# Kernel tuning notes

Hardware: AMD Instinct MI355X
Metric: run time of the kernel (lower is better)

## Reference

```python
import jax, jax.numpy as jnp
import numpy as np

B, C, N, M_MODES, EMB = 8, 64, 2048, 32, 256
MFREQ = 2 * M_MODES * (2 * M_MODES - 1)  # 4032
SCALE = 1.0 / (C * C)


def setup_inputs() -> dict:
    key = jax.random.key(0)
    ks = jax.random.split(key, 16)
    d = {
        "x": jax.random.normal(ks[0], (B, C, N), jnp.float32),
        "emb": jax.random.normal(ks[1], (B, EMB), jnp.float32),
        "Vf_re": jax.random.normal(ks[2], (MFREQ, N), jnp.float32),
        "Vf_im": jax.random.normal(ks[3], (MFREQ, N), jnp.float32),
        "Vi_re": jax.random.normal(ks[4], (N, MFREQ), jnp.float32),
        "Vi_im": jax.random.normal(ks[5], (N, MFREQ), jnp.float32),
        "w1_re": SCALE * jax.random.uniform(ks[6], (C, C, M_MODES, M_MODES), jnp.float32),
        "w1_im": SCALE * jax.random.uniform(ks[7], (C, C, M_MODES, M_MODES), jnp.float32),
        "w2_re": SCALE * jax.random.uniform(ks[8], (C, C, M_MODES, M_MODES), jnp.float32),
        "w2_im": SCALE * jax.random.uniform(ks[9], (C, C, M_MODES, M_MODES), jnp.float32),
        "m1_re": SCALE * jax.random.uniform(ks[10], (1, M_MODES, M_MODES, EMB), jnp.float32),
        "m1_im": SCALE * jax.random.uniform(ks[11], (1, M_MODES, M_MODES, EMB), jnp.float32),
        "m2_re": SCALE * jax.random.uniform(ks[12], (1, M_MODES, M_MODES, EMB), jnp.float32),
        "m2_im": SCALE * jax.random.uniform(ks[13], (1, M_MODES, M_MODES, EMB), jnp.float32),
    }
    return d


def _spectral_conv(x, emb, Vf, Vi, w1, w2, mod1, mod2):
    m = M_MODES
    # nuft.forward: [B,N,C] complex -> [B,MFREQ,C]
    xc = jnp.transpose(x, (0, 2, 1)).astype(jnp.complex64)
    x_nfft = jnp.einsum('mn,bnc->bmc', Vf, xc)
    # [B,C,2m,2m-1]
    x_ft = jnp.transpose(x_nfft, (0, 2, 1)).reshape(x.shape[0], C, 2 * m, 2 * m - 1)
    embc = emb.astype(jnp.complex64)[:, None, None, :]  # [B,1,1,EMB]
    phi1 = jnp.sum(mod1 * embc, axis=-1)  # [B,m,m]
    phi2 = jnp.sum(mod2 * embc, axis=-1)
    out1 = jnp.einsum('bixy,ioxy->boxy', x_ft[:, :, :m, :m], w1)
    out2 = jnp.einsum('bixy,ioxy->boxy', x_ft[:, :, -m:, :m], w2)
    mod1b = phi1[:, None, :, :] * out1
    mod2b = phi2[:, None, :, :] * out2
    out_ft = jnp.concatenate([mod1b, mod2b], axis=2)  # [B,C,2m,m]
    xf = out_ft.reshape(x.shape[0], C, 2 * m * m)
    # Hermitian-symmetry reconstruction: flip over mode AND channel dims, conj
    xf2 = jnp.conj(jnp.flip(xf[..., 2 * m:], axis=(-2, -1)))
    xf = jnp.concatenate([xf, xf2], axis=-1)  # [B,C,MFREQ]
    xf = jnp.transpose(xf, (0, 2, 1))  # [B,MFREQ,C]
    out = jnp.einsum('nm,bmc->bnc', Vi, xf)  # nuft.inverse -> [B,N,C]
    out = jnp.transpose(out, (0, 2, 1)) / N * 2
    return out.real


def reference(x, emb, Vf_re, Vf_im, Vi_re, Vi_im, w1_re, w1_im, w2_re, w2_im, m1_re, m1_im, m2_re, m2_im):
    Vf = Vf_re + 1j * Vf_im
    Vi = Vi_re + 1j * Vi_im
    w1 = w1_re + 1j * w1_im
    w2 = w2_re + 1j * w2_im
    mod1 = m1_re + 1j * m1_im
    mod2 = m2_re + 1j * m2_im
    return _spectral_conv(x, emb, Vf, Vi, w1, w2, mod1, mod2)
```

## Files before the change

### kernel.cpp

```cpp
#include <hip/hip_runtime.h>

#define BB    8
#define CC    64
#define NN    2048
#define GG    2048
#define MFREQ 4032

typedef __attribute__((ext_vector_type(4))) float f32x4;
typedef __attribute__((ext_vector_type(8))) short bf16x8;

static __device__ __forceinline__ unsigned short f2bf(float f) {
    union { float f; unsigned u; } v; v.f = f;
    unsigned r = v.u + 0x7fff + ((v.u >> 16) & 1);
    return (unsigned short)(r >> 16);
}

#define ASYNC_COPY16(gp, lp)                                                        \
    __builtin_amdgcn_global_load_lds(                                               \
        (const __attribute__((address_space(1))) unsigned int*)(gp),                \
        (__attribute__((address_space(3))) unsigned int*)(lp), 16, 0, 0)

__global__ __launch_bounds__(256) void prep_all(const float* __restrict__ vf_re,
                                                const float* __restrict__ vf_im,
                                                const float* __restrict__ x,
                                                const float* __restrict__ vi_re,
                                                const float* __restrict__ vi_im,
                                                const float* __restrict__ w1_re,
                                                const float* __restrict__ w1_im,
                                                const float* __restrict__ w2_re,
                                                const float* __restrict__ w2_im,
                                                const float* __restrict__ m1_re,
                                                const float* __restrict__ m1_im,
                                                const float* __restrict__ m2_re,
                                                const float* __restrict__ m2_im,
                                                const float* __restrict__ emb,
                                                unsigned short* __restrict__ af,
                                                unsigned short* __restrict__ xb,
                                                unsigned short* __restrict__ mi,
                                                unsigned int* __restrict__ wt,
                                                float* __restrict__ phi_re,
                                                float* __restrict__ phi_im) {
    __shared__ float sre[32][33];
    __shared__ float sim[32][33];
    __shared__ float sr4[4], si4[4];
    int blk = blockIdx.x;
    int t = threadIdx.x;

    if (blk < 6400) {
        float4 v[2][2];
        unsigned short* dst[2];
        if (blk < 2048) {
            #pragma unroll
            for (int u = 0; u < 2; ++u) {
                int gi = blk * 512 + u * 256 + t;
                int m = gi >> 8;
                int q8 = (gi & 255) * 8;
                int g = m & 2047;
                int f = (g >> 5) * 63 + (g & 31);
                const float* src = (m < 2048 ? vf_re : vf_im) + (size_t)f * 2048 + q8;
                v[u][0] = *(const float4*)src;
                v[u][1] = *(const float4*)(src + 4);
                dst[u] = af + (size_t)m * 2048 + q8;
            }
        } else if (blk < 2304) {
            #pragma unroll
            for (int u = 0; u < 2; ++u) {
                int gi = (blk - 2048) * 512 + u * 256 + t;
                int q8 = gi * 8;
                v[u][0] = *(const float4*)(x + q8);
                v[u][1] = *(const float4*)(x + q8 + 4);
                dst[u] = xb + q8;
            }
        } else {
            #pragma unroll
            for (int u = 0; u < 2; ++u) {
                int gi = (blk - 2304) * 512 + u * 256 + t;
                int n = gi >> 10;
                int q8 = (gi & 1023) * 8;
                int region = q8 >> 11;
                int off = q8 & 2047;
                if (region == 0) {
                    const float* src = vi_re + (size_t)n * MFREQ + off;
                    v[u][0] = *(const float4*)src;
                    v[u][1] = *(const float4*)(src + 4);
                } else if (region == 1) {
                    const float* src = vi_im + (size_t)n * MFREQ + off;
                    float4 a = *(const float4*)src;
                    float4 b = *(const float4*)(src + 4);
                    v[u][0].x = -a.x; v[u][0].y = -a.y; v[u][0].z = -a.z; v[u][0].w = -a.w;
                    v[u][1].x = -b.x; v[u][1].y = -b.y; v[u][1].z = -b.z; v[u][1].w = -b.w;
                } else {
                    if (off < 64) {
                        v[u][0].x = v[u][0].y = v[u][0].z = v[u][0].w = 0.0f;
                        v[u][1].x = v[u][1].y = v[u][1].z = v[u][1].w = 0.0f;
                    } else {
                        const float* src = (region == 2 ? vi_re : vi_im) + (size_t)n * MFREQ;
                        float4 a = *(const float4*)(src + 4092 - off);
                        float4 b = *(const float4*)(src + 4088 - off);
                        v[u][0].x = a.w; v[u][0].y = a.z; v[u][0].z = a.y; v[u][0].w = a.x;
                        v[u][1].x = b.w; v[u][1].y = b.z; v[u][1].z = b.y; v[u][1].w = b.x;
                    }
                }
                dst[u] = mi + (size_t)n * 8192 + q8;
            }
        }
        #pragma unroll
        for (int u = 0; u < 2; ++u) {
            uint4 o;
            o.x = (unsigned int)f2bf(v[u][0].x) | ((unsigned int)f2bf(v[u][0].y) << 16);
            o.y = (unsigned int)f2bf(v[u][0].z) | ((unsigned int)f2bf(v[u][0].w) << 16);
            o.z = (unsigned int)f2bf(v[u][1].x) | ((unsigned int)f2bf(v[u][1].y) << 16);
            o.w = (unsigned int)f2bf(v[u][1].z) | ((unsigned int)f2bf(v[u][1].w) << 16);
            *(uint4*)dst[u] = o;
        }
    } else if (blk < 14592) {
        int bi = blk - 6400;
        int wsel = bi >> 12;
        int bj = bi & 4095;
        int io0 = (bj >> 5) * 32;
        int xy0 = (bj & 31) * 32;
        const float* wre = wsel ? w2_re : w1_re;
        const float* wim = wsel ? w2_im : w1_im;
        int r = t >> 3, c4 = (t & 7) * 4;
        float4 a = *(const float4*)(wre + (size_t)(io0 + r) * 1024 + xy0 + c4);
        float4 b = *(const float4*)(wim + (size_t)(io0 + r) * 1024 + xy0 + c4);
        sre[r][c4 + 0] = a.x; sre[r][c4 + 1] = a.y; sre[r][c4 + 2] = a.z; sre[r][c4 + 3] = a.w;
        sim[r][c4 + 0] = b.x; sim[r][c4 + 1] = b.y; sim[r][c4 + 2] = b.z; sim[r][c4 + 3] = b.w;
        __syncthreads();
        int gr = t >> 3, ic4 = (t & 7) * 4;
        uint4 o;
        o.x = (unsigned int)f2bf(sre[ic4 + 0][gr]) | ((unsigned int)f2bf(sim[ic4 + 0][gr]) << 16);
        o.y = (unsigned int)f2bf(sre[ic4 + 1][gr]) | ((unsigned int)f2bf(sim[ic4 + 1][gr]) << 16);
        o.z = (unsigned int)f2bf(sre[ic4 + 2][gr]) | ((unsigned int)f2bf(sim[ic4 + 2][gr]) << 16);
        o.w = (unsigned int)f2bf(sre[ic4 + 3][gr]) | ((unsigned int)f2bf(sim[ic4 + 3][gr]) << 16);
        int g = xy0 + gr + wsel * 1024;
        *(uint4*)(wt + (size_t)g * 4096 + io0 + ic4) = o;
    } else {
        int g = blk - 14592, e = t;
        int xy = g & 1023;
        const float* mr = (g < 1024 ? m1_re : m2_re) + xy * 256;
        const float* mp = (g < 1024 ? m1_im : m2_im) + xy * 256;
        float vr = mr[e], vi = mp[e];
        for (int bb = 0; bb < 8; ++bb) {
            float em = emb[bb * 256 + e];
            float pr = vr * em, pi = vi * em;
            for (int s = 32; s > 0; s >>= 1) { pr += __shfl_down(pr, s); pi += __shfl_down(pi, s); }
            int wid = e >> 6;
            if ((e & 63) == 0) { sr4[wid] = pr; si4[wid] = pi; }
            __syncthreads();
            if (e == 0) {
                phi_re[bb * 2048 + g] = sr4[0] + sr4[1] + sr4[2] + sr4[3];
                phi_im[bb * 2048 + g] = si4[0] + si4[1] + si4[2] + si4[3];
            }
            __syncthreads();
        }
    }
}

template<int TM>
__global__ __launch_bounds__(256, 2) void gemm_sk(const unsigned short* __restrict__ A,
                                                  const unsigned short* __restrict__ Bm,
                                                  float* __restrict__ P,
                                                  int M, int N, int K, int Kper, int ilv) {
    constexpr int FI = TM / 32;
    __shared__ unsigned short As[TM * 64];
    __shared__ unsigned short Bs[TM * 64];
    int t = threadIdx.x;
    int lane = t & 63, w = t >> 6;
    int m0 = blockIdx.y * TM, n0 = blockIdx.x * TM;
    int z = blockIdx.z;
    int kbase = z * Kper;
    int wm = (w >> 1) * (TM / 2), wn = (w & 1) * (TM / 2);
    int lr = lane & 15, quad = lane >> 4;
    int rsub = lane >> 3, slot = lane & 7;

    f32x4 acc[FI][FI] = {};

    for (int kk = kbase; kk < kbase + Kper; kk += 64) {
        __syncthreads();
        #pragma unroll
        for (int l = 0; l < FI; ++l) {
            int r = (w * FI + l) * 8 + rsub;
            int c = slot ^ (r & 7);
            ASYNC_COPY16(A + (size_t)(m0 + r) * K + kk + c * 8, As + r * 64 + slot * 8);
            ASYNC_COPY16(Bm + (size_t)(n0 + r) * K + kk + c * 8, Bs + r * 64 + slot * 8);
        }
        __syncthreads();
        #pragma unroll
        for (int ks = 0; ks < 2; ++ks) {
            bf16x8 af[FI], bfr[FI];
            #pragma unroll
            for (int i = 0; i < FI; ++i) {
                int row = wm + i * 16 + lr;
                int q = (ks * 4 + quad) ^ (row & 7);
                af[i] = *(const bf16x8*)(As + row * 64 + q * 8);
                int rowb = wn + i * 16 + lr;
                int qb = (ks * 4 + quad) ^ (rowb & 7);
                bfr[i] = *(const bf16x8*)(Bs + rowb * 64 + qb * 8);
            }
            #pragma unroll
            for (int i = 0; i < FI; ++i)
            #pragma unroll
            for (int j = 0; j < FI; ++j)
                acc[i][j] = __builtin_amdgcn_mfma_f32_16x16x32_bf16(af[i], bfr[j], acc[i][j], 0, 0, 0);
        }
    }
    float* Pz = P + (size_t)z * M * N;
    size_t rstride = ilv ? 1024 : (size_t)N;
    #pragma unroll
    for (int i = 0; i < FI; ++i)
    #pragma unroll
    for (int j = 0; j < FI; ++j) {
        int rr = m0 + wm + i * 16 + quad * 4;
        int cc = n0 + wn + j * 16 + lr;
        size_t base = ilv ? ((size_t)(rr & 2047) * 1024 + cc * 2 + (rr >> 11))
                          : ((size_t)rr * N + cc);
        float* cp = Pz + base;
        f32x4 v = acc[i][j];
        cp[0]           = v.x;
        cp[rstride]     = v.y;
        cp[2 * rstride] = v.z;
        cp[3 * rstride] = v.w;
    }
}

__global__ __launch_bounds__(256) void reduce_k(const float* __restrict__ P,
                                                float* __restrict__ out,
                                                int S, size_t elems, float alpha) {
    size_t idx = ((size_t)blockIdx.x * 256 + threadIdx.x) * 4;
    float4 s = *(const float4*)(P + idx);
    for (int zz = 1; zz < S; ++zz) {
        float4 v = *(const float4*)(P + (size_t)zz * elems + idx);
        s.x += v.x; s.y += v.y; s.z += v.z; s.w += v.w;
    }
    s.x *= alpha; s.y *= alpha; s.z *= alpha; s.w *= alpha;
    *(float4*)(out + idx) = s;
}

__global__ __launch_bounds__(256, 4) void middle_k(const float* __restrict__ O1,
                                                   const unsigned int* __restrict__ wt,
                                                   const float* __restrict__ phi_re,
                                                   const float* __restrict__ phi_im,
                                                   unsigned short* __restrict__ Yt) {
    __shared__ unsigned int sW[2][4096];
    __shared__ float sInc[2][1024];
    int t = threadIdx.x;
    int g0 = blockIdx.x * 2;
    int b = t >> 5, p = t & 31;

    #pragma unroll
    for (int gt = 0; gt < 2; ++gt) {
        int g = g0 + gt;
        #pragma unroll
        for (int j = 0; j < 4; ++j)
            ASYNC_COPY16(wt + (size_t)g * 4096 + (j * 256 + t) * 4, &sW[gt][(j * 256 + t) * 4]);
        ASYNC_COPY16(O1 + (size_t)g * 1024 + t * 4, &sInc[gt][t * 4]);
    }
    __syncthreads();

    unsigned short reA[2][2], imA[2][2];

    #pragma unroll
    for (int gt = 0; gt < 2; ++gt) {
        int g = g0 + gt;
        float ar0 = 0.f, ai0 = 0.f, ar1 = 0.f, ai1 = 0.f;
        const float2* incp = (const float2*)sInc[gt] + b * 64;
        const unsigned int* wp = sW[gt] + 2 * p;
        #pragma unroll 8
        for (int i = 0; i < 64; ++i) {
            float2 a = incp[i];
            uint2 uu = *(const uint2*)(wp + i * 64);
            float w0r = __uint_as_float(uu.x << 16);
            float w0i = __uint_as_float(uu.x & 0xffff0000u);
            float w1r = __uint_as_float(uu.y << 16);
            float w1i = __uint_as_float(uu.y & 0xffff0000u);
            ar0 += a.x * w0r - a.y * w0i;  ai0 += a.x * w0i + a.y * w0r;
            ar1 += a.x * w1r - a.y * w1i;  ai1 += a.x * w1i + a.y * w1r;
        }
        float pr = phi_re[b * 2048 + g], pi = phi_im[b * 2048 + g];
        reA[0][gt] = f2bf(pr * ar0 - pi * ai0);
        imA[0][gt] = f2bf(pr * ai0 + pi * ar0);
        reA[1][gt] = f2bf(pr * ar1 - pi * ai1);
        imA[1][gt] = f2bf(pr * ai1 + pi * ar1);
    }

    #pragma unroll
    for (int ch = 0; ch < 2; ++ch) {
        int c = 2 * p + ch;
        size_t r0 = (size_t)(b * 64 + c) * 8192;
        size_t rf = (size_t)(b * 64 + 63 - c) * 8192;
        unsigned int ure = (unsigned int)reA[ch][0] | ((unsigned int)reA[ch][1] << 16);
        unsigned int uim = (unsigned int)imA[ch][0] | ((unsigned int)imA[ch][1] << 16);
        *(unsigned int*)(Yt + r0 + g0)        = ure;
        *(unsigned int*)(Yt + r0 + 2048 + g0) = uim;
        *(unsigned int*)(Yt + rf + 4096 + g0) = ure;
        *(unsigned int*)(Yt + rf + 6144 + g0) = uim;
    }
}

extern "C" void kernel_launch(void* const* d_in, const int* in_sizes, int n_in,
                              void* d_out, int out_size, void* d_ws, size_t ws_size,
                              hipStream_t stream) {
    const float* x     = (const float*)d_in[0];
    const float* emb   = (const float*)d_in[1];
    const float* vf_re = (const float*)d_in[2];
    const float* vf_im = (const float*)d_in[3];
    const float* vi_re = (const float*)d_in[4];
    const float* vi_im = (const float*)d_in[5];
    const float* w1_re = (const float*)d_in[6];
    const float* w1_im = (const float*)d_in[7];
    const float* w2_re = (const float*)d_in[8];
    const float* w2_im = (const float*)d_in[9];
    const float* m1_re = (const float*)d_in[10];
    const float* m1_im = (const float*)d_in[11];
    const float* m2_re = (const float*)d_in[12];
    const float* m2_im = (const float*)d_in[13];

    char* ws = (char*)d_ws;
    unsigned short* Af = (unsigned short*)(ws);
    unsigned short* Xb = (unsigned short*)(ws + 16777216);
    unsigned short* Mi = (unsigned short*)(ws + 18874368);
    unsigned int*   Wt = (unsigned int*)(ws + 52428800);
    float*          O1 = (float*)(ws + 85983232);
    float*       PhiRe = (float*)(ws + 94371840);
    float*       PhiIm = (float*)(ws + 94437376);
    unsigned short* Yt = (unsigned short*)(ws + 94502912);
    float*          P  = (float*)(ws + 102891520);
    float* out = (float*)d_out;

    prep_all<<<16640, 256, 0, stream>>>(vf_re, vf_im, x, vi_re, vi_im,
                                        w1_re, w1_im, w2_re, w2_im,
                                        m1_re, m1_im, m2_re, m2_im, emb,
                                        Af, Xb, Mi, Wt, PhiRe, PhiIm);

    gemm_sk<64><<<dim3(8, 64, 1), 256, 0, stream>>>(Af, Xb, O1, 4096, 512, 2048, 2048, 1);

    middle_k<<<1024, 256, 0, stream>>>(O1, Wt, PhiRe, PhiIm, Yt);

    gemm_sk<128><<<dim3(16, 4, 8), 256, 0, stream>>>(Yt, Mi, P, 512, 2048, 8192, 1024, 0);
    reduce_k<<<1024, 256, 0, stream>>>(P, out, 8, (size_t)512 * 2048, 1.0f / 1024.0f);
}
```

Baseline: 314.8 us.

## Grid-stride software-pipelined bf16 conversion and XCD-aware block remapping in GEMM

The conversion portion of prep_all now uses 1280 persistent-style blocks. Each thread processes 10 units with a grid stride, prefetching the next unit's loads before packing and storing the current one. This replaces 6400 blocks that each did two units. The GEMM kernel also remaps linear workgroup IDs so that consecutive tiles land on the same XCD (8 chiplets), aiming for better L2 reuse. The risks are lower parallelism in the prep phase and a dependence on the workgroup count being divisible by 8.

Measured after the change: 318.2 us. About the same (+1.1%).

```diff
diff --git a/kernel.cpp b/kernel.cpp
--- a/kernel.cpp
+++ b/kernel.cpp
@@ -15,10 +15,67 @@
     return (unsigned short)(r >> 16);
 }
 
+static __device__ __forceinline__ unsigned int pk2(float lo, float hi) {
+    return (unsigned int)f2bf(lo) | ((unsigned int)f2bf(hi) << 16);
+}
+
 #define ASYNC_COPY16(gp, lp)                                                        \
     __builtin_amdgcn_global_load_lds(                                               \
         (const __attribute__((address_space(1))) unsigned int*)(gp),                \
         (__attribute__((address_space(3))) unsigned int*)(lp), 16, 0, 0)
+
+static __device__ __forceinline__ void decode_unit(int uid,
+        const float* __restrict__ vf_re, const float* __restrict__ vf_im,
+        const float* __restrict__ x,
+        const float* __restrict__ vi_re, const float* __restrict__ vi_im,
+        unsigned short* __restrict__ af, unsigned short* __restrict__ xb,
+        unsigned short* __restrict__ mi,
+        const float*& pa, const float*& pb, unsigned short*& dst, int& mode) {
+    if (uid < 1048576) {
+        int m = uid >> 8;
+        int q8 = (uid & 255) * 8;
+        int g = m & 2047;
+        int f = (g >> 5) * 63 + (g & 31);
+        const float* src = (m < 2048 ? vf_re : vf_im) + (size_t)f * 2048 + q8;
+        pa = src; pb = src + 4; dst = af + (size_t)m * 2048 + q8; mode = 0;
+    } else if (uid < 1179648) {
+        int v = uid - 1048576;
+        int q8 = v * 8;
+        pa = x + q8; pb = x + q8 + 4; dst = xb + q8; mode = 0;
+    } else {
+        int v = uid - 1179648;
+        int n = v >> 10;
+        int q8 = (v & 1023) * 8;
+        int region = q8 >> 11;
+        int off = q8 & 2047;
+        dst = mi + (size_t)n * 8192 + q8;
+        if (region == 0) {
+            pa = vi_re + (size_t)n * MFREQ + off; pb = pa + 4; mode = 0;
+        } else if (region == 1) {
+            pa = vi_im + (size_t)n * MFREQ + off; pb = pa + 4; mode = 1;
+        } else {
+            const float* src = (region == 2 ? vi_re : vi_im) + (size_t)n * MFREQ;
+            if (off < 64) { pa = src; pb = src; mode = 3; }
+            else { pa = src + 4092 - off; pb = src + 4088 - off; mode = 2; }
+        }
+    }
+}
+
+static __device__ __forceinline__ uint4 pack_unit(float4 a, float4 b, int mode) {
+    uint4 o;
+    if (mode == 3) { o.x = o.y = o.z = o.w = 0u; return o; }
+    if (mode == 2) {
+        o.x = pk2(a.w, a.z); o.y = pk2(a.y, a.x);
+        o.z = pk2(b.w, b.z); o.w = pk2(b.y, b.x);
+    } else if (mode == 1) {
+        o.x = pk2(-a.x, -a.y); o.y = pk2(-a.z, -a.w);
+        o.z = pk2(-b.x, -b.y); o.w = pk2(-b.z, -b.w);
+    } else {
+        o.x = pk2(a.x, a.y); o.y = pk2(a.z, a.w);
+        o.z = pk2(b.x, b.y); o.w = pk2(b.z, b.w);
+    }
+    return o;
+}
 
 __global__ __launch_bounds__(256) void prep_all(const float* __restrict__ vf_re,
                                                 const float* __restrict__ vf_im,
@@ -46,75 +103,30 @@
     int blk = blockIdx.x;
     int t = threadIdx.x;
 
-    if (blk < 6400) {
-        float4 v[2][2];
-        unsigned short* dst[2];
-        if (blk < 2048) {
-            #pragma unroll
-            for (int u = 0; u < 2; ++u) {
-                int gi = blk * 512 + u * 256 + t;
-                int m = gi >> 8;
-                int q8 = (gi & 255) * 8;
-                int g = m & 2047;
-                int f = (g >> 5) * 63 + (g & 31);
-                const float* src = (m < 2048 ? vf_re : vf_im) + (size_t)f * 2048 + q8;
-                v[u][0] = *(const float4*)src;
-                v[u][1] = *(const float4*)(src + 4);
-                dst[u] = af + (size_t)m * 2048 + q8;
+    if (blk < 1280) {
+        const int STRIDE = 1280 * 256;
+        int uid0 = blk * 256 + t;
+        const float *pa0, *pb0; unsigned short* d0; int md0;
+        decode_unit(uid0, vf_re, vf_im, x, vi_re, vi_im, af, xb, mi, pa0, pb0, d0, md0);
+        float4 A0 = *(const float4*)pa0;
+        float4 B0 = *(const float4*)pb0;
+        #pragma unroll
+        for (int i = 1; i <= 10; ++i) {
+            const float *pa1 = pa0, *pb1 = pb0; unsigned short* d1 = d0; int md1 = md0;
+            float4 A1 = A0, B1 = B0;
+            if (i < 10) {
+                decode_unit(uid0 + i * STRIDE, vf_re, vf_im, x, vi_re, vi_im,
+                            af, xb, mi, pa1, pb1, d1, md1);
+                A1 = *(const float4*)pa1;
+                B1 = *(const float4*)pb1;
             }
-        } else if (blk < 2304) {
-            #pragma unroll
-            for (int u = 0; u < 2; ++u) {
-                int gi = (blk - 2048) * 512 + u * 256 + t;
-                int q8 = gi * 8;
-                v[u][0] = *(const float4*)(x + q8);
-                v[u][1] = *(const float4*)(x + q8 + 4);
-                dst[u] = xb + q8;
-            }
-        } else {
-            #pragma unroll
-            for (int u = 0; u < 2; ++u) {
-                int gi = (blk - 2304) * 512 + u * 256 + t;
-                int n = gi >> 10;
-                int q8 = (gi & 1023) * 8;
-                int region = q8 >> 11;
-                int off = q8 & 2047;
-                if (region == 0) {
-                    const float* src = vi_re + (size_t)n * MFREQ + off;
-                    v[u][0] = *(const float4*)src;
-                    v[u][1] = *(const float4*)(src + 4);
-                } else if (region == 1) {
-                    const float* src = vi_im + (size_t)n * MFREQ + off;
-                    float4 a = *(const float4*)src;
-                    float4 b = *(const float4*)(src + 4);
-                    v[u][0].x = -a.x; v[u][0].y = -a.y; v[u][0].z = -a.z; v[u][0].w = -a.w;
-                    v[u][1].x = -b.x; v[u][1].y = -b.y; v[u][1].z = -b.z; v[u][1].w = -b.w;
-                } else {
-                    if (off < 64) {
-                        v[u][0].x = v[u][0].y = v[u][0].z = v[u][0].w = 0.0f;
-                        v[u][1].x = v[u][1].y = v[u][1].z = v[u][1].w = 0.0f;
-                    } else {
-                        const float* src = (region == 2 ? vi_re : vi_im) + (size_t)n * MFREQ;
-                        float4 a = *(const float4*)(src + 4092 - off);
-                        float4 b = *(const float4*)(src + 4088 - off);
-                        v[u][0].x = a.w; v[u][0].y = a.z; v[u][0].z = a.y; v[u][0].w = a.x;
-                        v[u][1].x = b.w; v[u][1].y = b.z; v[u][1].z = b.y; v[u][1].w = b.x;
-                    }
-                }
-                dst[u] = mi + (size_t)n * 8192 + q8;
-            }
-        }
-        #pragma unroll
-        for (int u = 0; u < 2; ++u) {
-            uint4 o;
-            o.x = (unsigned int)f2bf(v[u][0].x) | ((unsigned int)f2bf(v[u][0].y) << 16);
-            o.y = (unsigned int)f2bf(v[u][0].z) | ((unsigned int)f2bf(v[u][0].w) << 16);
-            o.z = (unsigned int)f2bf(v[u][1].x) | ((unsigned int)f2bf(v[u][1].y) << 16);
-            o.w = (unsigned int)f2bf(v[u][1].z) | ((unsigned int)f2bf(v[u][1].w) << 16);
-            *(uint4*)dst[u] = o;
-        }
-    } else if (blk < 14592) {
-        int bi = blk - 6400;
+            uint4 o = pack_unit(A0, B0, md0);
+            *(uint4*)d0 = o;
+            A0 = A1; B0 = B1; d0 = d1; md0 = md1;
+            pa0 = pa1; pb0 = pb1;
+        }
+    } else if (blk < 9472) {
+        int bi = blk - 1280;
         int wsel = bi >> 12;
         int bj = bi & 4095;
         int io0 = (bj >> 5) * 32;
@@ -136,7 +148,7 @@
         int g = xy0 + gr + wsel * 1024;
         *(uint4*)(wt + (size_t)g * 4096 + io0 + ic4) = o;
     } else {
-        int g = blk - 14592, e = t;
+        int g = blk - 9472, e = t;
         int xy = g & 1023;
         const float* mr = (g < 1024 ? m1_re : m2_re) + xy * 256;
         const float* mp = (g < 1024 ? m1_im : m2_im) + xy * 256;
@@ -167,8 +179,17 @@
     __shared__ unsigned short Bs[TM * 64];
     int t = threadIdx.x;
     int lane = t & 63, w = t >> 6;
-    int m0 = blockIdx.y * TM, n0 = blockIdx.x * TM;
-    int z = blockIdx.z;
+
+    unsigned nx = gridDim.x, ny = gridDim.y;
+    unsigned nwg = nx * ny * gridDim.z;
+    unsigned orig = (blockIdx.z * ny + blockIdx.y) * nx + blockIdx.x;
+    unsigned cpx = nwg >> 3;
+    unsigned wid = (orig & 7) * cpx + (orig >> 3);
+    unsigned bx = wid % nx; unsigned rem = wid / nx;
+    unsigned by = rem % ny; unsigned bz = rem / ny;
+
+    int m0 = by * TM, n0 = bx * TM;
+    int z = bz;
     int kbase = z * Kper;
     int wm = (w >> 1) * (TM / 2), wn = (w & 1) * (TM / 2);
     int lr = lane & 15, quad = lane >> 4;
@@ -328,7 +349,7 @@
     float*          P  = (float*)(ws + 102891520);
     float* out = (float*)d_out;
 
-    prep_all<<<16640, 256, 0, stream>>>(vf_re, vf_im, x, vi_re, vi_im,
+    prep_all<<<11520, 256, 0, stream>>>(vf_re, vf_im, x, vi_re, vi_im,
                                         w1_re, w1_im, w2_re, w2_im,
                                         m1_re, m1_im, m2_re, m2_im, emb,
                                         Af, Xb, Mi, Wt, PhiRe, PhiIm);
```

## Fuse x and Vi bf16 conversion into GEMM B-operand loads

Applied to the files above, without the earlier changes.

Removes the prep passes that converted x and the Vi matrices (with negation, flip and zero padding) to bf16 workspace buffers. The two GEMMs now read the fp32 sources directly, convert to bf16 in registers and write them into LDS, in place of the async global-to-LDS copy. This cuts the extra global write and re-read of the large Mi buffer and the Xb buffer. In exchange the GEMM loads become synchronous fp32 loads carrying twice the bytes plus conversion work in the inner loop, and Vi is re-read by every M-tile block.

New measurement: 363.9 us. 1.16x slower.

```diff
diff --git a/kernel.cpp b/kernel.cpp
--- a/kernel.cpp
+++ b/kernel.cpp
@@ -15,6 +15,26 @@
     return (unsigned short)(r >> 16);
 }
 
+static __device__ __forceinline__ unsigned int pk2(float lo, float hi) {
+    return (unsigned int)f2bf(lo) | ((unsigned int)f2bf(hi) << 16);
+}
+
+static __device__ __forceinline__ uint4 pack_unit(float4 a, float4 b, int mode) {
+    uint4 o;
+    if (mode == 3) { o.x = o.y = o.z = o.w = 0u; return o; }
+    if (mode == 2) {
+        o.x = pk2(a.w, a.z); o.y = pk2(a.y, a.x);
+        o.z = pk2(b.w, b.z); o.w = pk2(b.y, b.x);
+    } else if (mode == 1) {
+        o.x = pk2(-a.x, -a.y); o.y = pk2(-a.z, -a.w);
+        o.z = pk2(-b.x, -b.y); o.w = pk2(-b.z, -b.w);
+    } else {
+        o.x = pk2(a.x, a.y); o.y = pk2(a.z, a.w);
+        o.z = pk2(b.x, b.y); o.w = pk2(b.z, b.w);
+    }
+    return o;
+}
+
 #define ASYNC_COPY16(gp, lp)                                                        \
     __builtin_amdgcn_global_load_lds(                                               \
         (const __attribute__((address_space(1))) unsigned int*)(gp),                \
@@ -22,9 +42,6 @@
 
 __global__ __launch_bounds__(256) void prep_all(const float* __restrict__ vf_re,
                                                 const float* __restrict__ vf_im,
-                                                const float* __restrict__ x,
-                                                const float* __restrict__ vi_re,
-                                                const float* __restrict__ vi_im,
                                                 const float* __restrict__ w1_re,
                                                 const float* __restrict__ w1_im,
                                                 const float* __restrict__ w2_re,
@@ -35,8 +52,6 @@
                                                 const float* __restrict__ m2_im,
                                                 const float* __restrict__ emb,
                                                 unsigned short* __restrict__ af,
-                                                unsigned short* __restrict__ xb,
-                                                unsigned short* __restrict__ mi,
                                                 unsigned int* __restrict__ wt,
                                                 float* __restrict__ phi_re,
                                                 float* __restrict__ phi_im) {
@@ -46,75 +61,21 @@
     int blk = blockIdx.x;
     int t = threadIdx.x;
 
-    if (blk < 6400) {
-        float4 v[2][2];
-        unsigned short* dst[2];
-        if (blk < 2048) {
-            #pragma unroll
-            for (int u = 0; u < 2; ++u) {
-                int gi = blk * 512 + u * 256 + t;
-                int m = gi >> 8;
-                int q8 = (gi & 255) * 8;
-                int g = m & 2047;
-                int f = (g >> 5) * 63 + (g & 31);
-                const float* src = (m < 2048 ? vf_re : vf_im) + (size_t)f * 2048 + q8;
-                v[u][0] = *(const float4*)src;
-                v[u][1] = *(const float4*)(src + 4);
-                dst[u] = af + (size_t)m * 2048 + q8;
-            }
-        } else if (blk < 2304) {
-            #pragma unroll
-            for (int u = 0; u < 2; ++u) {
-                int gi = (blk - 2048) * 512 + u * 256 + t;
-                int q8 = gi * 8;
-                v[u][0] = *(const float4*)(x + q8);
-                v[u][1] = *(const float4*)(x + q8 + 4);
-                dst[u] = xb + q8;
-            }
-        } else {
-            #pragma unroll
-            for (int u = 0; u < 2; ++u) {
-                int gi = (blk - 2304) * 512 + u * 256 + t;
-                int n = gi >> 10;
-                int q8 = (gi & 1023) * 8;
-                int region = q8 >> 11;
-                int off = q8 & 2047;
-                if (region == 0) {
-                    const float* src = vi_re + (size_t)n * MFREQ + off;
-                    v[u][0] = *(const float4*)src;
-                    v[u][1] = *(const float4*)(src + 4);
-                } else if (region == 1) {
-                    const float* src = vi_im + (size_t)n * MFREQ + off;
-                    float4 a = *(const float4*)src;
-                    float4 b = *(const float4*)(src + 4);
-                    v[u][0].x = -a.x; v[u][0].y = -a.y; v[u][0].z = -a.z; v[u][0].w = -a.w;
-                    v[u][1].x = -b.x; v[u][1].y = -b.y; v[u][1].z = -b.z; v[u][1].w = -b.w;
-                } else {
-                    if (off < 64) {
-                        v[u][0].x = v[u][0].y = v[u][0].z = v[u][0].w = 0.0f;
-                        v[u][1].x = v[u][1].y = v[u][1].z = v[u][1].w = 0.0f;
-                    } else {
-                        const float* src = (region == 2 ? vi_re : vi_im) + (size_t)n * MFREQ;
-                        float4 a = *(const float4*)(src + 4092 - off);
-                        float4 b = *(const float4*)(src + 4088 - off);
-                        v[u][0].x = a.w; v[u][0].y = a.z; v[u][0].z = a.y; v[u][0].w = a.x;
-                        v[u][1].x = b.w; v[u][1].y = b.z; v[u][1].z = b.y; v[u][1].w = b.x;
-                    }
-                }
-                dst[u] = mi + (size_t)n * 8192 + q8;
-            }
-        }
+    if (blk < 2048) {
         #pragma unroll
         for (int u = 0; u < 2; ++u) {
-            uint4 o;
-            o.x = (unsigned int)f2bf(v[u][0].x) | ((unsigned int)f2bf(v[u][0].y) << 16);
-            o.y = (unsigned int)f2bf(v[u][0].z) | ((unsigned int)f2bf(v[u][0].w) << 16);
-            o.z = (unsigned int)f2bf(v[u][1].x) | ((unsigned int)f2bf(v[u][1].y) << 16);
-            o.w = (unsigned int)f2bf(v[u][1].z) | ((unsigned int)f2bf(v[u][1].w) << 16);
-            *(uint4*)dst[u] = o;
-        }
-    } else if (blk < 14592) {
-        int bi = blk - 6400;
+            int gi = blk * 512 + u * 256 + t;
+            int m = gi >> 8;
+            int q8 = (gi & 255) * 8;
+            int g = m & 2047;
+            int f = (g >> 5) * 63 + (g & 31);
+            const float* src = (m < 2048 ? vf_re : vf_im) + (size_t)f * 2048 + q8;
+            float4 a = *(const float4*)src;
+            float4 b = *(const float4*)(src + 4);
+            *(uint4*)(af + (size_t)m * 2048 + q8) = pack_unit(a, b, 0);
+        }
+    } else if (blk < 10240) {
+        int bi = blk - 2048;
         int wsel = bi >> 12;
         int bj = bi & 4095;
         int io0 = (bj >> 5) * 32;
@@ -136,7 +97,7 @@
         int g = xy0 + gr + wsel * 1024;
         *(uint4*)(wt + (size_t)g * 4096 + io0 + ic4) = o;
     } else {
-        int g = blk - 14592, e = t;
+        int g = blk - 10240, e = t;
         int xy = g & 1023;
         const float* mr = (g < 1024 ? m1_re : m2_re) + xy * 256;
         const float* mp = (g < 1024 ? m1_im : m2_im) + xy * 256;
@@ -157,9 +118,10 @@
     }
 }
 
-template<int TM>
+template<int TM, int BMODE>
 __global__ __launch_bounds__(256, 2) void gemm_sk(const unsigned short* __restrict__ A,
-                                                  const unsigned short* __restrict__ Bm,
+                                                  const float* __restrict__ Bf1,
+                                                  const float* __restrict__ Bf2,
                                                   float* __restrict__ P,
                                                   int M, int N, int K, int Kper, int ilv) {
     constexpr int FI = TM / 32;
@@ -183,7 +145,30 @@
             int r = (w * FI + l) * 8 + rsub;
             int c = slot ^ (r & 7);
             ASYNC_COPY16(A + (size_t)(m0 + r) * K + kk + c * 8, As + r * 64 + slot * 8);
-            ASYNC_COPY16(Bm + (size_t)(n0 + r) * K + kk + c * 8, Bs + r * 64 + slot * 8);
+            int q8 = kk + c * 8;
+            if constexpr (BMODE == 1) {
+                const float* src = Bf1 + (size_t)(n0 + r) * 2048 + q8;
+                float4 a = *(const float4*)src;
+                float4 b = *(const float4*)(src + 4);
+                *(uint4*)(Bs + r * 64 + slot * 8) = pack_unit(a, b, 0);
+            } else {
+                int n = n0 + r;
+                int region = q8 >> 11;
+                int off = q8 & 2047;
+                const float *pa, *pb; int mode;
+                if (region == 0) {
+                    pa = Bf1 + (size_t)n * MFREQ + off; pb = pa + 4; mode = 0;
+                } else if (region == 1) {
+                    pa = Bf2 + (size_t)n * MFREQ + off; pb = pa + 4; mode = 1;
+                } else {
+                    const float* src = (region == 2 ? Bf1 : Bf2) + (size_t)n * MFREQ;
+                    if (off < 64) { pa = src; pb = src; mode = 3; }
+                    else { pa = src + 4092 - off; pb = src + 4088 - off; mode = 2; }
+                }
+                float4 a = *(const float4*)pa;
+                float4 b = *(const float4*)pb;
+                *(uint4*)(Bs + r * 64 + slot * 8) = pack_unit(a, b, mode);
+            }
         }
         __syncthreads();
         #pragma unroll
@@ -318,8 +303,6 @@
 
     char* ws = (char*)d_ws;
     unsigned short* Af = (unsigned short*)(ws);
-    unsigned short* Xb = (unsigned short*)(ws + 16777216);
-    unsigned short* Mi = (unsigned short*)(ws + 18874368);
     unsigned int*   Wt = (unsigned int*)(ws + 52428800);
     float*          O1 = (float*)(ws + 85983232);
     float*       PhiRe = (float*)(ws + 94371840);
@@ -328,15 +311,17 @@
     float*          P  = (float*)(ws + 102891520);
     float* out = (float*)d_out;
 
-    prep_all<<<16640, 256, 0, stream>>>(vf_re, vf_im, x, vi_re, vi_im,
+    prep_all<<<12288, 256, 0, stream>>>(vf_re, vf_im,
                                         w1_re, w1_im, w2_re, w2_im,
                                         m1_re, m1_im, m2_re, m2_im, emb,
-                                        Af, Xb, Mi, Wt, PhiRe, PhiIm);
-
-    gemm_sk<64><<<dim3(8, 64, 1), 256, 0, stream>>>(Af, Xb, O1, 4096, 512, 2048, 2048, 1);
+                                        Af, Wt, PhiRe, PhiIm);
+
+    gemm_sk<64, 1><<<dim3(8, 64, 1), 256, 0, stream>>>(Af, x, nullptr, O1,
+                                                       4096, 512, 2048, 2048, 1);
 
     middle_k<<<1024, 256, 0, stream>>>(O1, Wt, PhiRe, PhiIm, Yt);
 
-    gemm_sk<128><<<dim3(16, 4, 8), 256, 0, stream>>>(Yt, Mi, P, 512, 2048, 8192, 1024, 0);
+    gemm_sk<128, 2><<<dim3(16, 4, 8), 256, 0, stream>>>(Yt, vi_re, vi_im, P,
+                                                        512, 2048, 8192, 1024, 0);
     reduce_k<<<1024, 256, 0, stream>>>(P, out, 8, (size_t)512 * 2048, 1.0f / 1024.0f);
 }
```
